# Kernel optimization log

Hardware: AMD Instinct MI355X
Metric: run time of the kernel (lower is better)

## Reference

```python
import jax, jax.numpy as jnp
import numpy as np

IGNORE_INDEX = -100


def setup_inputs() -> dict:
    key = jax.random.key(0)
    k1, k2, k3 = jax.random.split(key, 3)
    BT, H, V = 4096, 2048, 32000
    hidden_states = jax.random.normal(k1, (BT, H), dtype=jnp.float32) * 0.02
    weight = jax.random.normal(k2, (V, H), dtype=jnp.float32) * 0.02
    targets = jax.random.randint(k3, (BT,), 0, V, dtype=jnp.int64)
    return {"hidden_states": hidden_states, "weight": weight, "targets": targets}


def reference(hidden_states, weight, targets):
    # Fused lm_head projection + cross-entropy with ignore_index masking,
    # 'mean' reduction over valid rows (matches reduction='mean').
    logits = jnp.einsum('bh,vh->bv', hidden_states, weight).astype(jnp.float32)  # (BT, V)
    lse = jax.nn.logsumexp(logits, axis=-1)  # (BT,)
    safe_tgt = jnp.clip(targets, 0, logits.shape[-1] - 1)
    target_logit = jnp.take_along_axis(logits, safe_tgt[:, None], axis=-1)[:, 0]
    valid = targets != IGNORE_INDEX
    loss_rows = jnp.where(valid, lse - target_logit, 0.0)  # (BT,)
    n_valid = jnp.maximum(valid.sum(), 1)
    return loss_rows.sum() / n_valid.astype(jnp.float32)
```

## Files before the change

### kernel.cpp

```cpp
#include <hip/hip_runtime.h>

#define BT 4096
#define H  2048
#define V  32000
#define BM 256
#define BN 256
#define BKB 128
#define KT (H / BKB)
#define NTILES (V / BN)
#define MTILES (BT / BM)
#define NWG (MTILES * NTILES)
#define IGNORE_INDEX (-100)

typedef int   v8i   __attribute__((ext_vector_type(8)));
typedef float f32x4 __attribute__((ext_vector_type(4)));

#define SCALE_ONE 0x7F7F7F7F
#define UNSCALE   (1.0f / 65536.0f)

#define BAR()   __builtin_amdgcn_s_barrier()
#define SB0()   __builtin_amdgcn_sched_barrier(0)
#define LGKM0() asm volatile("s_waitcnt lgkmcnt(0)" ::: "memory")
#define VMC(N)  asm volatile("s_waitcnt vmcnt(" #N ")" ::: "memory")

__device__ inline void load_lds16(const void* g, void* l) {
  __builtin_amdgcn_global_load_lds(
      (const __attribute__((address_space(1))) unsigned int*)g,
      (__attribute__((address_space(3))) unsigned int*)l,
      16, 0, 0);
}

__global__ __launch_bounds__(256)
void cvt_pack_kernel(const float* __restrict__ in, unsigned char* __restrict__ out,
                     int tasks) {
  __shared__ float ld[4][16][132];
  const int wv = threadIdx.x >> 6, lane = threadIdx.x & 63;
  const int task = blockIdx.x * 4 + wv;
  if (task >= tasks) return;
  const int g = task >> 4, kt = task & 15;
  const float* src = in + (size_t)(g * 16) * H + kt * 128;
#pragma unroll
  for (int i = 0; i < 8; ++i) {
    int idx = i * 64 + lane;
    int r = idx >> 5, c = idx & 31;
    float4 v = *(const float4*)(src + (size_t)r * H + c * 4);
    *(float4*)&ld[wv][r][c * 4] = v;
  }
  LGKM0();
  const int row = lane & 15, kb = (lane >> 4) * 32;
  int p[8];
#pragma unroll
  for (int u = 0; u < 8; ++u) {
    float4 x = *(const float4*)&ld[wv][row][kb + u * 4];
    int v = 0;
    v = __builtin_amdgcn_cvt_pk_fp8_f32(x.x * 256.f, x.y * 256.f, v, false);
    v = __builtin_amdgcn_cvt_pk_fp8_f32(x.z * 256.f, x.w * 256.f, v, true);
    p[u] = v;
  }
  unsigned char* dst = out + ((size_t)g * KT + kt) * 2048 + lane * 16;
  int4 lo; lo.x = p[0]; lo.y = p[1]; lo.z = p[2]; lo.w = p[3];
  int4 hi; hi.x = p[4]; hi.y = p[5]; hi.z = p[6]; hi.w = p[7];
  *(int4*)dst          = lo;
  *(int4*)(dst + 1024) = hi;
}

union frag_u { v8i v; int4 h[2]; };

#define MF(C, A, B)                                                         \
  (C) = __builtin_amdgcn_mfma_scale_f32_16x16x128_f8f6f4(                   \
      (A).v, (B).v, (C), 0, 0, 0, SCALE_ONE, 0, SCALE_ONE)

__global__ __launch_bounds__(512, 2)
void gemm_lse_kernel(const unsigned char* __restrict__ Af8,
                     const unsigned char* __restrict__ Bf8,
                     const int* __restrict__ tgt,
                     float* __restrict__ pm, float* __restrict__ pl,
                     float* __restrict__ tl) {
  __shared__ __align__(16) unsigned char As[2 * 32768];
  __shared__ __align__(16) unsigned char Bs[2 * 32768];
  __shared__ float red_m[4][BM];
  __shared__ float red_l[4][BM];
  __shared__ int   stgt[BM];

  const int wgid = ((int)blockIdx.x & 7) * (NWG / 8) + ((int)blockIdx.x >> 3);
  const int mt = wgid & (MTILES - 1);
  const int nt = wgid / MTILES;
  const int m0 = mt * BM;
  const int n0 = nt * BN;

  const int tid  = threadIdx.x;
  const int lane = tid & 63;
  const int w    = tid >> 6;
  const int wr   = w >> 2;
  const int wc   = w & 3;
  const int lm   = lane & 15;
  const int q    = lane >> 4;

  if (tid < BM) stgt[tid] = tgt[m0 + tid];
  __syncthreads();

  const unsigned char* aSrc = Af8 + (size_t)(m0 / 16) * KT * 2048;
  const unsigned char* bSrc = Bf8 + (size_t)(n0 / 16) * KT * 2048;

  auto stageA = [&](int buf, int hf, int kt) {
    const unsigned char* s = aSrc + ((size_t)(hf * 8 + w) * KT + kt) * 2048;
    unsigned char* d = As + buf * 32768 + (hf * 8 + w) * 2048;
    load_lds16(s, d);
    load_lds16(s + 1024, d + 1024);
  };
  auto stageB = [&](int buf, int hf, int kt) {
    const unsigned char* s = bSrc + ((size_t)(hf * 8 + w) * KT + kt) * 2048;
    unsigned char* d = Bs + buf * 32768 + (hf * 8 + w) * 2048;
    load_lds16(s, d);
    load_lds16(s + 1024, d + 1024);
  };

  const unsigned char* aRd = As + lane * 16;
  const unsigned char* bRd = Bs + lane * 16;

  auto ldA = [&](frag_u& f, int buf, int i) {
    const unsigned char* p = aRd + buf * 32768 + (wr * 8 + i) * 2048;
    f.h[0] = *(const int4*)(p);
    f.h[1] = *(const int4*)(p + 1024);
  };
  auto ldB = [&](frag_u& f, int buf, int j) {
    const unsigned char* p = bRd + buf * 32768 + (wc * 4 + j) * 2048;
    f.h[0] = *(const int4*)(p);
    f.h[1] = *(const int4*)(p + 1024);
  };

  f32x4 acc[8][4];
#pragma unroll
  for (int a = 0; a < 8; ++a)
#pragma unroll
    for (int b = 0; b < 4; ++b) acc[a][b] = (f32x4){0.f, 0.f, 0.f, 0.f};

  frag_u fa0, fa1, fa2, fa3, fb0, fb1, fb2, fb3;

  stageA(0, 0, 0); stageA(0, 1, 0); stageB(0, 0, 0); stageB(0, 1, 0);
  stageB(1, 0, 1); stageB(1, 1, 1);
  VMC(4);
  SB0(); BAR(); SB0();

  for (int i = 0; i < 8; ++i) {
    const int t1 = 2 * i + 1;
    const bool pre = (i < 7);

    ldA(fa0, 0, 0); ldA(fa1, 0, 1); ldA(fa2, 0, 2); ldA(fa3, 0, 3);
    ldB(fb0, 0, 0); ldB(fb1, 0, 1); ldB(fb2, 0, 2); ldB(fb3, 0, 3);
    stageA(1, 0, t1); stageA(1, 1, t1);
    __builtin_amdgcn_s_setprio(1);
    MF(acc[0][0], fa0, fb0); MF(acc[1][0], fa1, fb0);
    MF(acc[2][0], fa2, fb0); MF(acc[3][0], fa3, fb0);
    MF(acc[0][1], fa0, fb1); MF(acc[1][1], fa1, fb1);
    MF(acc[2][1], fa2, fb1); MF(acc[3][1], fa3, fb1);
    MF(acc[0][2], fa0, fb2); MF(acc[1][2], fa1, fb2);
    MF(acc[2][2], fa2, fb2); MF(acc[3][2], fa3, fb2);
    MF(acc[0][3], fa0, fb3); MF(acc[1][3], fa1, fb3);
    MF(acc[2][3], fa2, fb3); MF(acc[3][3], fa3, fb3);
    __builtin_amdgcn_s_setprio(0);
    SB0(); BAR(); SB0();

    ldA(fa0, 0, 4); ldA(fa1, 0, 5); ldA(fa2, 0, 6); ldA(fa3, 0, 7);
    if (pre) { stageB(0, 0, 2 * i + 2); stageB(0, 1, 2 * i + 2); }
    __builtin_amdgcn_s_setprio(1);
    MF(acc[4][0], fa0, fb0); MF(acc[5][0], fa1, fb0);
    MF(acc[6][0], fa2, fb0); MF(acc[7][0], fa3, fb0);
    MF(acc[4][1], fa0, fb1); MF(acc[5][1], fa1, fb1);
    MF(acc[6][1], fa2, fb1); MF(acc[7][1], fa3, fb1);
    MF(acc[4][2], fa0, fb2); MF(acc[5][2], fa1, fb2);
    MF(acc[6][2], fa2, fb2); MF(acc[7][2], fa3, fb2);
    MF(acc[4][3], fa0, fb3); MF(acc[5][3], fa1, fb3);
    MF(acc[6][3], fa2, fb3); MF(acc[7][3], fa3, fb3);
    __builtin_amdgcn_s_setprio(0);
    if (pre) { VMC(4); } else { VMC(0); }
    SB0(); BAR(); SB0();

    ldA(fa0, 1, 0); ldA(fa1, 1, 1); ldA(fa2, 1, 2); ldA(fa3, 1, 3);
    ldB(fb0, 1, 0); ldB(fb1, 1, 1); ldB(fb2, 1, 2); ldB(fb3, 1, 3);
    if (pre) { stageA(0, 0, 2 * i + 2); stageA(0, 1, 2 * i + 2); }
    __builtin_amdgcn_s_setprio(1);
    MF(acc[0][0], fa0, fb0); MF(acc[1][0], fa1, fb0);
    MF(acc[2][0], fa2, fb0); MF(acc[3][0], fa3, fb0);
    MF(acc[0][1], fa0, fb1); MF(acc[1][1], fa1, fb1);
    MF(acc[2][1], fa2, fb1); MF(acc[3][1], fa3, fb1);
    MF(acc[0][2], fa0, fb2); MF(acc[1][2], fa1, fb2);
    MF(acc[2][2], fa2, fb2); MF(acc[3][2], fa3, fb2);
    MF(acc[0][3], fa0, fb3); MF(acc[1][3], fa1, fb3);
    MF(acc[2][3], fa2, fb3); MF(acc[3][3], fa3, fb3);
    __builtin_amdgcn_s_setprio(0);
    SB0(); BAR(); SB0();

    ldA(fa0, 1, 4); ldA(fa1, 1, 5); ldA(fa2, 1, 6); ldA(fa3, 1, 7);
    if (pre) { stageB(1, 0, t1 + 2); stageB(1, 1, t1 + 2); }
    __builtin_amdgcn_s_setprio(1);
    MF(acc[4][0], fa0, fb0); MF(acc[5][0], fa1, fb0);
    MF(acc[6][0], fa2, fb0); MF(acc[7][0], fa3, fb0);
    MF(acc[4][1], fa0, fb1); MF(acc[5][1], fa1, fb1);
    MF(acc[6][1], fa2, fb1); MF(acc[7][1], fa3, fb1);
    MF(acc[4][2], fa0, fb2); MF(acc[5][2], fa1, fb2);
    MF(acc[6][2], fa2, fb2); MF(acc[7][2], fa3, fb2);
    MF(acc[4][3], fa0, fb3); MF(acc[5][3], fa1, fb3);
    MF(acc[6][3], fa2, fb3); MF(acc[7][3], fa3, fb3);
    __builtin_amdgcn_s_setprio(0);
    if (pre) { VMC(4); } else { VMC(0); }
    SB0(); BAR(); SB0();
  }

  __syncthreads();

#pragma unroll
  for (int ai = 0; ai < 8; ++ai) {
#pragma unroll
    for (int r = 0; r < 4; ++r) {
      int row_local = wr * 128 + ai * 16 + q * 4 + r;
      int c = stgt[row_local] - n0 - wc * 64;
      if ((unsigned)c < 64u && (c & 15) == lm) {
        int bj = c >> 4;
        float v = bj == 0 ? acc[ai][0][r]
                : bj == 1 ? acc[ai][1][r]
                : bj == 2 ? acc[ai][2][r]
                :           acc[ai][3][r];
        tl[m0 + row_local] = v * UNSCALE;
      }
    }
  }

#pragma unroll
  for (int ai = 0; ai < 8; ++ai) {
#pragma unroll
    for (int r = 0; r < 4; ++r) {
      float v0 = acc[ai][0][r] * UNSCALE;
      float v1 = acc[ai][1][r] * UNSCALE;
      float v2 = acc[ai][2][r] * UNSCALE;
      float v3 = acc[ai][3][r] * UNSCALE;
      float mx = fmaxf(fmaxf(v0, v1), fmaxf(v2, v3));
#pragma unroll
      for (int off = 1; off < 16; off <<= 1) mx = fmaxf(mx, __shfl_xor(mx, off));
      float s = __expf(v0 - mx) + __expf(v1 - mx) + __expf(v2 - mx) + __expf(v3 - mx);
#pragma unroll
      for (int off = 1; off < 16; off <<= 1) s += __shfl_xor(s, off);
      if (lm == 0) {
        int row_local = wr * 128 + ai * 16 + q * 4 + r;
        red_m[wc][row_local] = mx;
        red_l[wc][row_local] = s;
      }
    }
  }
  __syncthreads();
  if (tid < BM) {
    float M = fmaxf(fmaxf(red_m[0][tid], red_m[1][tid]),
                    fmaxf(red_m[2][tid], red_m[3][tid]));
    float L = red_l[0][tid] * __expf(red_m[0][tid] - M)
            + red_l[1][tid] * __expf(red_m[1][tid] - M)
            + red_l[2][tid] * __expf(red_m[2][tid] - M)
            + red_l[3][tid] * __expf(red_m[3][tid] - M);
    long idx = (long)nt * BT + (m0 + tid);
    pm[idx] = M;
    pl[idx] = L;
  }
}

__global__ __launch_bounds__(256)
void row_lse_kernel(const float* __restrict__ pm, const float* __restrict__ pl,
                    const float* __restrict__ tl, const int* __restrict__ tgt,
                    float* __restrict__ rl) {
  int row  = blockIdx.x * 4 + (threadIdx.x >> 6);
  int lane = threadIdx.x & 63;
  float M = -__builtin_inff();
  float L = 0.f;
  for (int t = lane; t < NTILES; t += 64) {
    float m2 = pm[(long)t * BT + row];
    float l2 = pl[(long)t * BT + row];
    float Mn = fmaxf(M, m2);
    L = L * __expf(M - Mn) + l2 * __expf(m2 - Mn);
    M = Mn;
  }
#pragma unroll
  for (int off = 1; off < 64; off <<= 1) {
    float m2 = __shfl_xor(M, off);
    float l2 = __shfl_xor(L, off);
    float Mn = fmaxf(M, m2);
    L = L * __expf(M - Mn) + l2 * __expf(m2 - Mn);
    M = Mn;
  }
  if (lane == 0) {
    float lse = M + logf(L);
    int t = tgt[row];
    rl[row] = (t != IGNORE_INDEX) ? (lse - tl[row]) : 0.f;
  }
}

__global__ __launch_bounds__(256)
void final_kernel(const float* __restrict__ rl, const int* __restrict__ tgt,
                  float* __restrict__ out) {
  __shared__ float ss[4];
  __shared__ float sc[4];
  float s = 0.f, c = 0.f;
  for (int r = threadIdx.x; r < BT; r += 256) {
    s += rl[r];
    c += (tgt[r] != IGNORE_INDEX) ? 1.f : 0.f;
  }
#pragma unroll
  for (int off = 32; off > 0; off >>= 1) {
    s += __shfl_xor(s, off);
    c += __shfl_xor(c, off);
  }
  int w = threadIdx.x >> 6;
  if ((threadIdx.x & 63) == 0) { ss[w] = s; sc[w] = c; }
  __syncthreads();
  if (threadIdx.x == 0) {
    float S = ss[0] + ss[1] + ss[2] + ss[3];
    float C = sc[0] + sc[1] + sc[2] + sc[3];
    out[0] = S / fmaxf(C, 1.f);
  }
}

extern "C" void kernel_launch(void* const* d_in, const int* in_sizes, int n_in,
                              void* d_out, int out_size, void* d_ws, size_t ws_size,
                              hipStream_t stream) {
  const float* hs  = (const float*)d_in[0];
  const float* wt  = (const float*)d_in[1];
  const int*   tgt = (const int*)d_in[2];
  float*       out = (float*)d_out;

  char* ws = (char*)d_ws;
  size_t off = 0;
  auto alloc = [&](size_t bytes) -> void* {
    void* p = ws + off;
    off += (bytes + 255) & ~(size_t)255;
    return p;
  };
  unsigned char* wf8 = (unsigned char*)alloc((size_t)V * H);
  unsigned char* hf8 = (unsigned char*)alloc((size_t)BT * H);
  float* pm = (float*)alloc((size_t)NTILES * BT * 4);
  float* pl = (float*)alloc((size_t)NTILES * BT * 4);
  float* tl = (float*)alloc((size_t)BT * 4);
  float* rl = (float*)alloc((size_t)BT * 4);
  (void)ws_size; (void)in_sizes; (void)n_in; (void)out_size;

  cvt_pack_kernel<<<(V / 16) * KT / 4, 256, 0, stream>>>(wt, wf8, (V / 16) * KT);
  cvt_pack_kernel<<<(BT / 16) * KT / 4, 256, 0, stream>>>(hs, hf8, (BT / 16) * KT);

  gemm_lse_kernel<<<NWG, 512, 0, stream>>>(hf8, wf8, tgt, pm, pl, tl);

  row_lse_kernel<<<BT / 4, 256, 0, stream>>>(pm, pl, tl, tgt, rl);
  final_kernel<<<1, 256, 0, stream>>>(rl, tgt, out);
}
```

Measured before the change: 724.0 us.

## Single-buffer LDS and raise occupancy target to four workgroups per CU

Replaces the double-buffered LDS pipeline with one LDS buffer per operand, with loads issued after a barrier at the end of each K step. Launch bounds now ask for 4 workgroups of 512 threads per CU. The aim is to hide global-load latency through more resident waves rather than software prefetch. The risks are that the loads are now fully serialized with compute inside each workgroup, and that the tighter register budget may cause spills for the 32 accumulator fragments.

New measurement: 2.579 ms. 256% more time.

```diff
diff --git a/kernel.cpp b/kernel.cpp
--- a/kernel.cpp
+++ b/kernel.cpp
@@ -70,14 +70,14 @@
   (C) = __builtin_amdgcn_mfma_scale_f32_16x16x128_f8f6f4(                   \
       (A).v, (B).v, (C), 0, 0, 0, SCALE_ONE, 0, SCALE_ONE)
 
-__global__ __launch_bounds__(512, 2)
+__global__ __launch_bounds__(512, 4)
 void gemm_lse_kernel(const unsigned char* __restrict__ Af8,
                      const unsigned char* __restrict__ Bf8,
                      const int* __restrict__ tgt,
                      float* __restrict__ pm, float* __restrict__ pl,
                      float* __restrict__ tl) {
-  __shared__ __align__(16) unsigned char As[2 * 32768];
-  __shared__ __align__(16) unsigned char Bs[2 * 32768];
+  __shared__ __align__(16) unsigned char As[32768];
+  __shared__ __align__(16) unsigned char Bs[32768];
   __shared__ float red_m[4][BM];
   __shared__ float red_l[4][BM];
   __shared__ int   stgt[BM];
@@ -102,15 +102,15 @@
   const unsigned char* aSrc = Af8 + (size_t)(m0 / 16) * KT * 2048;
   const unsigned char* bSrc = Bf8 + (size_t)(n0 / 16) * KT * 2048;
 
-  auto stageA = [&](int buf, int hf, int kt) {
+  auto stageA = [&](int hf, int kt) {
     const unsigned char* s = aSrc + ((size_t)(hf * 8 + w) * KT + kt) * 2048;
-    unsigned char* d = As + buf * 32768 + (hf * 8 + w) * 2048;
+    unsigned char* d = As + (hf * 8 + w) * 2048;
     load_lds16(s, d);
     load_lds16(s + 1024, d + 1024);
   };
-  auto stageB = [&](int buf, int hf, int kt) {
+  auto stageB = [&](int hf, int kt) {
     const unsigned char* s = bSrc + ((size_t)(hf * 8 + w) * KT + kt) * 2048;
-    unsigned char* d = Bs + buf * 32768 + (hf * 8 + w) * 2048;
+    unsigned char* d = Bs + (hf * 8 + w) * 2048;
     load_lds16(s, d);
     load_lds16(s + 1024, d + 1024);
   };
@@ -118,13 +118,13 @@
   const unsigned char* aRd = As + lane * 16;
   const unsigned char* bRd = Bs + lane * 16;
 
-  auto ldA = [&](frag_u& f, int buf, int i) {
-    const unsigned char* p = aRd + buf * 32768 + (wr * 8 + i) * 2048;
+  auto ldA = [&](frag_u& f, int i) {
+    const unsigned char* p = aRd + (wr * 8 + i) * 2048;
     f.h[0] = *(const int4*)(p);
     f.h[1] = *(const int4*)(p + 1024);
   };
-  auto ldB = [&](frag_u& f, int buf, int j) {
-    const unsigned char* p = bRd + buf * 32768 + (wc * 4 + j) * 2048;
+  auto ldB = [&](frag_u& f, int j) {
+    const unsigned char* p = bRd + (wc * 4 + j) * 2048;
     f.h[0] = *(const int4*)(p);
     f.h[1] = *(const int4*)(p + 1024);
   };
@@ -137,18 +137,15 @@
 
   frag_u fa0, fa1, fa2, fa3, fb0, fb1, fb2, fb3;
 
-  stageA(0, 0, 0); stageA(0, 1, 0); stageB(0, 0, 0); stageB(0, 1, 0);
-  stageB(1, 0, 1); stageB(1, 1, 1);
-  VMC(4);
-  SB0(); BAR(); SB0();
-
-  for (int i = 0; i < 8; ++i) {
-    const int t1 = 2 * i + 1;
-    const bool pre = (i < 7);
-
-    ldA(fa0, 0, 0); ldA(fa1, 0, 1); ldA(fa2, 0, 2); ldA(fa3, 0, 3);
-    ldB(fb0, 0, 0); ldB(fb1, 0, 1); ldB(fb2, 0, 2); ldB(fb3, 0, 3);
-    stageA(1, 0, t1); stageA(1, 1, t1);
+  stageA(0, 0); stageA(1, 0); stageB(0, 0); stageB(1, 0);
+
+#pragma unroll 1
+  for (int kt = 0; kt < KT; ++kt) {
+    VMC(0);
+    SB0(); BAR(); SB0();
+
+    ldA(fa0, 0); ldA(fa1, 1); ldA(fa2, 2); ldA(fa3, 3);
+    ldB(fb0, 0); ldB(fb1, 1); ldB(fb2, 2); ldB(fb3, 3);
     __builtin_amdgcn_s_setprio(1);
     MF(acc[0][0], fa0, fb0); MF(acc[1][0], fa1, fb0);
     MF(acc[2][0], fa2, fb0); MF(acc[3][0], fa3, fb0);
@@ -159,10 +156,7 @@
     MF(acc[0][3], fa0, fb3); MF(acc[1][3], fa1, fb3);
     MF(acc[2][3], fa2, fb3); MF(acc[3][3], fa3, fb3);
     __builtin_amdgcn_s_setprio(0);
-    SB0(); BAR(); SB0();
-
-    ldA(fa0, 0, 4); ldA(fa1, 0, 5); ldA(fa2, 0, 6); ldA(fa3, 0, 7);
-    if (pre) { stageB(0, 0, 2 * i + 2); stageB(0, 1, 2 * i + 2); }
+    ldA(fa0, 4); ldA(fa1, 5); ldA(fa2, 6); ldA(fa3, 7);
     __builtin_amdgcn_s_setprio(1);
     MF(acc[4][0], fa0, fb0); MF(acc[5][0], fa1, fb0);
     MF(acc[6][0], fa2, fb0); MF(acc[7][0], fa3, fb0);
@@ -173,38 +167,14 @@
     MF(acc[4][3], fa0, fb3); MF(acc[5][3], fa1, fb3);
     MF(acc[6][3], fa2, fb3); MF(acc[7][3], fa3, fb3);
     __builtin_amdgcn_s_setprio(0);
-    if (pre) { VMC(4); } else { VMC(0); }
+
+    LGKM0();
     SB0(); BAR(); SB0();
 
-    ldA(fa0, 1, 0); ldA(fa1, 1, 1); ldA(fa2, 1, 2); ldA(fa3, 1, 3);
-    ldB(fb0, 1, 0); ldB(fb1, 1, 1); ldB(fb2, 1, 2); ldB(fb3, 1, 3);
-    if (pre) { stageA(0, 0, 2 * i + 2); stageA(0, 1, 2 * i + 2); }
-    __builtin_amdgcn_s_setprio(1);
-    MF(acc[0][0], fa0, fb0); MF(acc[1][0], fa1, fb0);
-    MF(acc[2][0], fa2, fb0); MF(acc[3][0], fa3, fb0);
-    MF(acc[0][1], fa0, fb1); MF(acc[1][1], fa1, fb1);
-    MF(acc[2][1], fa2, fb1); MF(acc[3][1], fa3, fb1);
-    MF(acc[0][2], fa0, fb2); MF(acc[1][2], fa1, fb2);
-    MF(acc[2][2], fa2, fb2); MF(acc[3][2], fa3, fb2);
-    MF(acc[0][3], fa0, fb3); MF(acc[1][3], fa1, fb3);
-    MF(acc[2][3], fa2, fb3); MF(acc[3][3], fa3, fb3);
-    __builtin_amdgcn_s_setprio(0);
-    SB0(); BAR(); SB0();
-
-    ldA(fa0, 1, 4); ldA(fa1, 1, 5); ldA(fa2, 1, 6); ldA(fa3, 1, 7);
-    if (pre) { stageB(1, 0, t1 + 2); stageB(1, 1, t1 + 2); }
-    __builtin_amdgcn_s_setprio(1);
-    MF(acc[4][0], fa0, fb0); MF(acc[5][0], fa1, fb0);
-    MF(acc[6][0], fa2, fb0); MF(acc[7][0], fa3, fb0);
-    MF(acc[4][1], fa0, fb1); MF(acc[5][1], fa1, fb1);
-    MF(acc[6][1], fa2, fb1); MF(acc[7][1], fa3, fb1);
-    MF(acc[4][2], fa0, fb2); MF(acc[5][2], fa1, fb2);
-    MF(acc[6][2], fa2, fb2); MF(acc[7][2], fa3, fb2);
-    MF(acc[4][3], fa0, fb3); MF(acc[5][3], fa1, fb3);
-    MF(acc[6][3], fa2, fb3); MF(acc[7][3], fa3, fb3);
-    __builtin_amdgcn_s_setprio(0);
-    if (pre) { VMC(4); } else { VMC(0); }
-    SB0(); BAR(); SB0();
+    if (kt + 1 < KT) {
+      stageA(0, kt + 1); stageA(1, kt + 1);
+      stageB(0, kt + 1); stageB(1, kt + 1);
+    }
   }
 
   __syncthreads();
```
